# Kernel optimization log

Measured on AMD Instinct MI355X. Metric: run time of the kernel, lower is better.

## Reference

```python
import jax, jax.numpy as jnp
import numpy as np

NUM_EMBEDDINGS = 16384
EMBED_DIM = 256
COMMITMENT_COST = 0.25  # legacy=True: vq_loss = commit + beta * codebook


def setup_inputs() -> dict:
    key = jax.random.key(0)
    k1, k2, k3, k4 = jax.random.split(key, 4)
    z = jax.random.normal(k1, (8, 2048, EMBED_DIM), dtype=jnp.float32)
    # frozen codebook: normal(0, embedding_dim ** -0.5)
    codebook = jax.random.normal(k2, (NUM_EMBEDDINGS, EMBED_DIM), dtype=jnp.float32) * (EMBED_DIM ** -0.5)
    # learnable linear projection, torch default uniform init
    bound = 1.0 / np.sqrt(EMBED_DIM)
    proj_w = jax.random.uniform(k3, (EMBED_DIM, EMBED_DIM), dtype=jnp.float32, minval=-bound, maxval=bound)
    proj_b = jax.random.uniform(k4, (EMBED_DIM,), dtype=jnp.float32, minval=-bound, maxval=bound)
    return {"z": z, "codebook": codebook, "proj_w": proj_w, "proj_b": proj_b}


def reference(z, codebook, proj_w, proj_b):
    B, T, D = z.shape
    # projected codebook (the only learned part of the quantizer)
    quant_codebook = codebook @ proj_w.T + proj_b  # [K, D]
    z_flat = z.reshape(-1, D)  # [N, D]
    # squared L2 distances: ||z||^2 + ||c||^2 - 2 z.c
    dists = (
        jnp.sum(z_flat * z_flat, axis=1, keepdims=True)
        + jnp.sum(quant_codebook * quant_codebook, axis=1)
        - 2.0 * jnp.einsum("nd,kd->nk", z_flat, quant_codebook)
    )  # [N, K]
    idx = jnp.argmin(dists, axis=1)  # [N]
    quantized = quant_codebook[idx].reshape(z.shape)  # [B, T, D]

    commitment_loss = jnp.mean((jax.lax.stop_gradient(quantized) - z) ** 2)
    codebook_loss = jnp.mean((quantized - jax.lax.stop_gradient(z)) ** 2)
    vq_loss = commitment_loss + COMMITMENT_COST * codebook_loss  # legacy formulation

    # straight-through estimator
    quantized = z + jax.lax.stop_gradient(quantized - z)
    encoding_indices = idx.reshape(B, T)
    return quantized, vq_loss, encoding_indices
```

## Files before the change

### kernel.cpp

```cpp
#include <hip/hip_runtime.h>

typedef unsigned short u16;
typedef __bf16 bf16x8 __attribute__((ext_vector_type(8)));
typedef float f32x4 __attribute__((ext_vector_type(4)));

#define NQ 16384
#define NC 16384
#define DD 256
#define BM 128
#define BN 256
#define BK 32
#define NSPLIT 4
#define NPART (NSPLIT * 2)
#define NTILES ((NC / NSPLIT) / BN)

__device__ __forceinline__ u16 f2bf(float x) {
  unsigned u = __float_as_uint(x);
  u += 0x7fffu + ((u >> 16) & 1u);
  return (u16)(u >> 16);
}
__device__ __forceinline__ float bf2f(u16 h) {
  return __uint_as_float(((unsigned)h) << 16);
}

__device__ __forceinline__ void gl2lds16(const void* g, void* l) {
  __builtin_amdgcn_global_load_lds((__attribute__((address_space(1))) void*)g,
                                   (__attribute__((address_space(3))) void*)l,
                                   16, 0, 0);
}

__global__ __launch_bounds__(256) void split_z_kernel(const float* __restrict__ z,
                                                      u16* __restrict__ Ah,
                                                      u16* __restrict__ Al) {
  size_t i = (size_t)blockIdx.x * 256 + threadIdx.x;
  float4 v = ((const float4*)z)[i];
  float f[4] = {v.x, v.y, v.z, v.w};
  u16 hh[4], ll[4];
#pragma unroll
  for (int j = 0; j < 4; ++j) {
    hh[j] = f2bf(f[j]);
    ll[j] = f2bf(f[j] - bf2f(hh[j]));
  }
  ushort4 h; h.x = hh[0]; h.y = hh[1]; h.z = hh[2]; h.w = hh[3];
  ushort4 l; l.x = ll[0]; l.y = ll[1]; l.z = ll[2]; l.w = ll[3];
  ((ushort4*)Ah)[i] = h;
  ((ushort4*)Al)[i] = l;
}

__global__ __launch_bounds__(256) void norm256_kernel(const float* __restrict__ x,
                                                      float* __restrict__ nrm) {
  const int t = threadIdx.x;
  const int j = t & 7;
  const int row = blockIdx.x * 32 + (t >> 3);
  const float* q = x + (size_t)row * 256;
  float half[2];
#pragma unroll
  for (int h = 0; h < 2; ++h) {
    const float* p = q + h * 128;
    float v0 = p[j];
    float r = __fmul_rn(v0, v0);
#pragma unroll
    for (int i = 8; i < 128; i += 8) {
      float v = p[i + j];
      r = __fadd_rn(r, __fmul_rn(v, v));
    }
    float s1 = __fadd_rn(r, __shfl_xor(r, 1));
    float s2 = __fadd_rn(s1, __shfl_xor(s1, 2));
    half[h] = __fadd_rn(s2, __shfl_xor(s2, 4));
  }
  if (j == 0) nrm[row] = __fadd_rn(half[0], half[1]);
}

__global__ __launch_bounds__(256) void qc_gemm_kernel(const float* __restrict__ cb,
                                                      const float* __restrict__ W,
                                                      const float* __restrict__ bias,
                                                      float* __restrict__ qc) {
  __shared__ float As[64][33];
  __shared__ float Bs[64][33];
  const int bm = blockIdx.x >> 2;
  const int bn = blockIdx.x & 3;
  const int m0 = bm * 64, n0 = bn * 64;
  const int t = threadIdx.x;
  const int tx = t & 15, ty = t >> 4;
  float acc[4][4] = {};
  for (int kc = 0; kc < 256; kc += 32) {
    __syncthreads();
#pragma unroll
    for (int j = 0; j < 8; ++j) {
      int idx = j * 256 + t;
      int r = idx >> 5, c = idx & 31;
      As[r][c] = cb[(size_t)(m0 + r) * 256 + kc + c];
      Bs[r][c] = W[(size_t)(n0 + r) * 256 + kc + c];
    }
    __syncthreads();
#pragma unroll
    for (int kk = 0; kk < 32; ++kk) {
      float a[4], b[4];
#pragma unroll
      for (int u = 0; u < 4; ++u) a[u] = As[ty * 4 + u][kk];
#pragma unroll
      for (int v = 0; v < 4; ++v) b[v] = Bs[tx * 4 + v][kk];
#pragma unroll
      for (int u = 0; u < 4; ++u)
#pragma unroll
        for (int v = 0; v < 4; ++v) acc[u][v] += a[u] * b[v];
    }
  }
#pragma unroll
  for (int u = 0; u < 4; ++u)
#pragma unroll
    for (int v = 0; v < 4; ++v) {
      int r = m0 + ty * 4 + u, c = n0 + tx * 4 + v;
      qc[(size_t)r * 256 + c] = acc[u][v] + bias[c];
    }
}

__global__ __launch_bounds__(256) void split_qc_kernel(const float* __restrict__ qc,
                                                       u16* __restrict__ Bh,
                                                       u16* __restrict__ Bl) {
  size_t i = (size_t)blockIdx.x * 256 + threadIdx.x;
  float4 v = ((const float4*)qc)[i];
  float f[4] = {v.x, v.y, v.z, v.w};
  u16 hh[4], ll[4];
#pragma unroll
  for (int j = 0; j < 4; ++j) {
    hh[j] = f2bf(f[j]);
    ll[j] = f2bf(f[j] - bf2f(hh[j]));
  }
  ushort4 h; h.x = hh[0]; h.y = hh[1]; h.z = hh[2]; h.w = hh[3];
  ushort4 l; l.x = ll[0]; l.y = ll[1]; l.z = ll[2]; l.w = ll[3];
  ((ushort4*)Bh)[i] = h;
  ((ushort4*)Bl)[i] = l;
}

__global__ __launch_bounds__(256, 2) void vq_argmin_kernel(
    const u16* __restrict__ Ah, const u16* __restrict__ Al,
    const u16* __restrict__ Bh, const u16* __restrict__ Bl,
    const float* __restrict__ cnorm, const float* __restrict__ znorm,
    float* __restrict__ pval, int* __restrict__ pidx) {
  __shared__ __align__(16) u16 Ahs[BM * BK];
  __shared__ __align__(16) u16 Als[BM * BK];
  __shared__ __align__(16) u16 Bhs[BN * BK];
  __shared__ __align__(16) u16 Bls[BN * BK];

  const int bm = blockIdx.x / NSPLIT;
  const int spl = blockIdx.x % NSPLIT;
  const int lane = threadIdx.x & 63;
  const int wid = threadIdx.x >> 6;
  const int wm = wid >> 1, wn = wid & 1;
  const int l15 = lane & 15;
  const int lg = lane >> 4;
  const int m0 = bm * BM;
  const int ns0 = spl * (NC / NSPLIT);

  const int st_r = lane >> 2;
  const int st_k = (((lane & 3) ^ ((lane >> 3) & 3)) << 3);

  const int rd_sw = ((lg ^ ((l15 >> 1) & 3)) << 3);

  float zrow[4][4];
#pragma unroll
  for (int mi = 0; mi < 4; ++mi)
#pragma unroll
    for (int i = 0; i < 4; ++i)
      zrow[mi][i] = znorm[m0 + wm * 64 + mi * 16 + lg * 4 + i];

  float rmin[4][4];
  int ridx[4][4];
#pragma unroll
  for (int a = 0; a < 4; ++a)
#pragma unroll
    for (int b = 0; b < 4; ++b) { rmin[a][b] = 3.4e38f; ridx[a][b] = 0; }

  for (int nt = 0; nt < NTILES; ++nt) {
    const int n0 = ns0 + nt * BN;
    f32x4 acc[4][8];
#pragma unroll
    for (int a = 0; a < 4; ++a)
#pragma unroll
      for (int b = 0; b < 8; ++b) {
        f32x4 zz = {0.f, 0.f, 0.f, 0.f};
        acc[a][b] = zz;
      }

    for (int kc = 0; kc < DD; kc += BK) {
      __syncthreads();
#pragma unroll
      for (int j = 0; j < 2; ++j) {
        const int grp = wid * 2 + j;
        const int r = grp * 16 + st_r;
        const size_t ga = (size_t)(m0 + r) * DD + kc + st_k;
        gl2lds16(Ah + ga, Ahs + grp * 512);
        gl2lds16(Al + ga, Als + grp * 512);
      }
#pragma unroll
      for (int j = 0; j < 4; ++j) {
        const int grp = wid * 4 + j;
        const int r = grp * 16 + st_r;
        const size_t gb = (size_t)(n0 + r) * DD + kc + st_k;
        gl2lds16(Bh + gb, Bhs + grp * 512);
        gl2lds16(Bl + gb, Bls + grp * 512);
      }
      __syncthreads();

      bf16x8 ah[4], al[4];
#pragma unroll
      for (int mi = 0; mi < 4; ++mi) {
        const int r = wm * 64 + mi * 16 + l15;
        const int off = r * BK + rd_sw;
        ah[mi] = *(const bf16x8*)&Ahs[off];
        al[mi] = *(const bf16x8*)&Als[off];
      }
#pragma unroll
      for (int ni = 0; ni < 8; ++ni) {
        const int r = wn * 128 + ni * 16 + l15;
        const int off = r * BK + rd_sw;
        const bf16x8 bh = *(const bf16x8*)&Bhs[off];
        const bf16x8 bl = *(const bf16x8*)&Bls[off];
#pragma unroll
        for (int mi = 0; mi < 4; ++mi) {
          acc[mi][ni] = __builtin_amdgcn_mfma_f32_16x16x32_bf16(ah[mi], bh, acc[mi][ni], 0, 0, 0);
          acc[mi][ni] = __builtin_amdgcn_mfma_f32_16x16x32_bf16(ah[mi], bl, acc[mi][ni], 0, 0, 0);
          acc[mi][ni] = __builtin_amdgcn_mfma_f32_16x16x32_bf16(al[mi], bh, acc[mi][ni], 0, 0, 0);
        }
      }
    }
#pragma unroll
    for (int ni = 0; ni < 8; ++ni) {
      const int col = n0 + wn * 128 + ni * 16 + l15;
      const float cn = cnorm[col];
#pragma unroll
      for (int mi = 0; mi < 4; ++mi)
#pragma unroll
        for (int i = 0; i < 4; ++i) {
          const float s = __fadd_rn(zrow[mi][i], cn);
          const float v = __fsub_rn(s, __fmul_rn(2.0f, acc[mi][ni][i]));
          if (v < rmin[mi][i]) { rmin[mi][i] = v; ridx[mi][i] = col; }
        }
    }
  }
#pragma unroll
  for (int mi = 0; mi < 4; ++mi)
#pragma unroll
    for (int i = 0; i < 4; ++i) {
      float v = rmin[mi][i];
      int ix = ridx[mi][i];
#pragma unroll
      for (int d = 1; d < 16; d <<= 1) {
        float ov = __shfl_xor(v, d);
        int oi = __shfl_xor(ix, d);
        if (ov < v || (ov == v && oi < ix)) { v = ov; ix = oi; }
      }
      if (l15 == 0) {
        const int row = m0 + wm * 64 + mi * 16 + lg * 4 + i;
        const int part = spl * 2 + wn;
        pval[(size_t)part * NQ + row] = v;
        pidx[(size_t)part * NQ + row] = ix;
      }
    }
}

__global__ __launch_bounds__(256) void finalize_kernel(
    const float* __restrict__ pval, const int* __restrict__ pidx,
    const float* __restrict__ qc, const float* __restrict__ z,
    float* __restrict__ out, float* __restrict__ loss_acc) {
  __shared__ int sidx[8];
  __shared__ float red[256];
  const int bid = blockIdx.x;
  const int t = threadIdx.x;
  if (t < 8) {
    const int row = bid * 8 + t;
    float best = pval[row];
    int bi = pidx[row];
    for (int s2 = 1; s2 < NPART; ++s2) {
      float v = pval[(size_t)s2 * NQ + row];
      int ix = pidx[(size_t)s2 * NQ + row];
      if (v < best || (v == best && ix < bi)) { best = v; bi = ix; }
    }
    sidx[t] = bi;
    out[4194305 + row] = (float)bi;
  }
  __syncthreads();
  float d2 = 0.f;
#pragma unroll
  for (int r = 0; r < 8; ++r) {
    const int row = bid * 8 + r;
    const int ix = sidx[r];
    const float q = qc[(size_t)ix * 256 + t];
    const float zz = z[(size_t)row * 256 + t];
    out[(size_t)row * 256 + t] = q;
    const float d = q - zz;
    d2 += d * d;
  }
  red[t] = d2;
  for (int st = 128; st; st >>= 1) {
    __syncthreads();
    if (t < st) red[t] += red[t + st];
  }
  if (t == 0) atomicAdd(loss_acc, red[0]);
}

__global__ void write_loss_kernel(const float* __restrict__ loss_acc, float* __restrict__ out) {
  out[4194304] = 1.25f * loss_acc[0] / 4194304.0f;
}

extern "C" void kernel_launch(void* const* d_in, const int* in_sizes, int n_in,
                              void* d_out, int out_size, void* d_ws, size_t ws_size,
                              hipStream_t stream) {
  const float* z = (const float*)d_in[0];
  const float* cb = (const float*)d_in[1];
  const float* W = (const float*)d_in[2];
  const float* bias = (const float*)d_in[3];
  float* out = (float*)d_out;
  char* ws = (char*)d_ws;

  constexpr size_t OFF_QC = 0;
  constexpr size_t OFF_AH = OFF_QC + 16777216;
  constexpr size_t OFF_AL = OFF_AH + 8388608;
  constexpr size_t OFF_BH = OFF_AL + 8388608;
  constexpr size_t OFF_BL = OFF_BH + 8388608;
  constexpr size_t OFF_CN = OFF_BL + 8388608;
  constexpr size_t OFF_ZN = OFF_CN + 65536;
  constexpr size_t OFF_PV = OFF_ZN + 65536;
  constexpr size_t OFF_PI = OFF_PV + 1048576;
  constexpr size_t OFF_ACC = OFF_PI + 1048576;

  float* qc = (float*)(ws + OFF_QC);
  u16* Ah = (u16*)(ws + OFF_AH);
  u16* Al = (u16*)(ws + OFF_AL);
  u16* Bh = (u16*)(ws + OFF_BH);
  u16* Bl = (u16*)(ws + OFF_BL);
  float* cn = (float*)(ws + OFF_CN);
  float* zn = (float*)(ws + OFF_ZN);
  float* pv = (float*)(ws + OFF_PV);
  int* pi = (int*)(ws + OFF_PI);
  float* lacc = (float*)(ws + OFF_ACC);

  hipMemsetAsync(lacc, 0, 4, stream);
  split_z_kernel<<<4096, 256, 0, stream>>>(z, Ah, Al);
  qc_gemm_kernel<<<1024, 256, 0, stream>>>(cb, W, bias, qc);
  norm256_kernel<<<NQ / 32, 256, 0, stream>>>(z, zn);
  norm256_kernel<<<NC / 32, 256, 0, stream>>>(qc, cn);
  split_qc_kernel<<<4096, 256, 0, stream>>>(qc, Bh, Bl);
  vq_argmin_kernel<<<(NQ / BM) * NSPLIT, 256, 0, stream>>>(Ah, Al, Bh, Bl, cn, zn, pv, pi);
  finalize_kernel<<<NQ / 8, 256, 0, stream>>>(pv, pi, qc, z, out, lacc);
  write_loss_kernel<<<1, 1, 0, stream>>>(lacc, out);
}
```

Before: 573.9 us.

## Double-buffer LDS tiles with async prefetch and regroup MFMA issue order

Adds two LDS buffers so the global-to-LDS loads for the next K-step are issued before computing the current one, which removes one barrier per step and overlaps memory with MFMA. The three split-precision MFMA passes are regrouped into separate loops over all B fragments, which are now held in registers. The split count drops from 4 to 2 and launch bounds change to 1 block per SM. That gives fewer but longer blocks, and znorm is reloaded per tile instead of kept in registers. Doubling LDS and the register pressure from the B fragments reduce occupancy, and fewer blocks may underfill the CUs.

New measurement: 680.9 us. 18.6% more time.

```diff
diff --git a/kernel.cpp b/kernel.cpp
--- a/kernel.cpp
+++ b/kernel.cpp
@@ -10,9 +10,10 @@
 #define BM 128
 #define BN 256
 #define BK 32
-#define NSPLIT 4
+#define NSPLIT 2
 #define NPART (NSPLIT * 2)
 #define NTILES ((NC / NSPLIT) / BN)
+#define NSTEPS (NTILES * 8)
 
 __device__ __forceinline__ u16 f2bf(float x) {
   unsigned u = __float_as_uint(x);
@@ -133,15 +134,15 @@
   ((ushort4*)Bl)[i] = l;
 }
 
-__global__ __launch_bounds__(256, 2) void vq_argmin_kernel(
+__global__ __launch_bounds__(256, 1) void vq_argmin_kernel(
     const u16* __restrict__ Ah, const u16* __restrict__ Al,
     const u16* __restrict__ Bh, const u16* __restrict__ Bl,
     const float* __restrict__ cnorm, const float* __restrict__ znorm,
     float* __restrict__ pval, int* __restrict__ pidx) {
-  __shared__ __align__(16) u16 Ahs[BM * BK];
-  __shared__ __align__(16) u16 Als[BM * BK];
-  __shared__ __align__(16) u16 Bhs[BN * BK];
-  __shared__ __align__(16) u16 Bls[BN * BK];
+  __shared__ __align__(16) u16 Ahs[2][BM * BK];
+  __shared__ __align__(16) u16 Als[2][BM * BK];
+  __shared__ __align__(16) u16 Bhs[2][BN * BK];
+  __shared__ __align__(16) u16 Bls[2][BN * BK];
 
   const int bm = blockIdx.x / NSPLIT;
   const int spl = blockIdx.x % NSPLIT;
@@ -158,12 +159,27 @@
 
   const int rd_sw = ((lg ^ ((l15 >> 1) & 3)) << 3);
 
-  float zrow[4][4];
-#pragma unroll
-  for (int mi = 0; mi < 4; ++mi)
-#pragma unroll
-    for (int i = 0; i < 4; ++i)
-      zrow[mi][i] = znorm[m0 + wm * 64 + mi * 16 + lg * 4 + i];
+  auto stage = [&](int buf, int s) {
+    const int ntt = s >> 3;
+    const int kcc = (s & 7) * BK;
+    const int nn0 = ns0 + ntt * BN;
+#pragma unroll
+    for (int j = 0; j < 2; ++j) {
+      const int grp = wid * 2 + j;
+      const int r = grp * 16 + st_r;
+      const size_t ga = (size_t)(m0 + r) * DD + kcc + st_k;
+      gl2lds16(Ah + ga, &Ahs[buf][grp * 512]);
+      gl2lds16(Al + ga, &Als[buf][grp * 512]);
+    }
+#pragma unroll
+    for (int j = 0; j < 4; ++j) {
+      const int grp = wid * 4 + j;
+      const int r = grp * 16 + st_r;
+      const size_t gb = (size_t)(nn0 + r) * DD + kcc + st_k;
+      gl2lds16(Bh + gb, &Bhs[buf][grp * 512]);
+      gl2lds16(Bl + gb, &Bls[buf][grp * 512]);
+    }
+  };
 
   float rmin[4][4];
   int ridx[4][4];
@@ -171,6 +187,9 @@
   for (int a = 0; a < 4; ++a)
 #pragma unroll
     for (int b = 0; b < 4; ++b) { rmin[a][b] = 3.4e38f; ridx[a][b] = 0; }
+
+  stage(0, 0);
+  __syncthreads();
 
   for (int nt = 0; nt < NTILES; ++nt) {
     const int n0 = ns0 + nt * BN;
@@ -183,60 +202,67 @@
         acc[a][b] = zz;
       }
 
-    for (int kc = 0; kc < DD; kc += BK) {
-      __syncthreads();
-#pragma unroll
-      for (int j = 0; j < 2; ++j) {
-        const int grp = wid * 2 + j;
-        const int r = grp * 16 + st_r;
-        const size_t ga = (size_t)(m0 + r) * DD + kc + st_k;
-        gl2lds16(Ah + ga, Ahs + grp * 512);
-        gl2lds16(Al + ga, Als + grp * 512);
-      }
-#pragma unroll
-      for (int j = 0; j < 4; ++j) {
-        const int grp = wid * 4 + j;
-        const int r = grp * 16 + st_r;
-        const size_t gb = (size_t)(n0 + r) * DD + kc + st_k;
-        gl2lds16(Bh + gb, Bhs + grp * 512);
-        gl2lds16(Bl + gb, Bls + grp * 512);
-      }
-      __syncthreads();
-
-      bf16x8 ah[4], al[4];
+#pragma unroll 1
+    for (int k8 = 0; k8 < 8; ++k8) {
+      const int s = nt * 8 + k8;
+      const int cur = s & 1;
+      if (s + 1 < NSTEPS) stage(cur ^ 1, s + 1);
+
+      bf16x8 ah[4], al[4], bh[8], bl[8];
 #pragma unroll
       for (int mi = 0; mi < 4; ++mi) {
         const int r = wm * 64 + mi * 16 + l15;
         const int off = r * BK + rd_sw;
-        ah[mi] = *(const bf16x8*)&Ahs[off];
-        al[mi] = *(const bf16x8*)&Als[off];
+        ah[mi] = *(const bf16x8*)&Ahs[cur][off];
+        al[mi] = *(const bf16x8*)&Als[cur][off];
       }
 #pragma unroll
       for (int ni = 0; ni < 8; ++ni) {
         const int r = wn * 128 + ni * 16 + l15;
         const int off = r * BK + rd_sw;
-        const bf16x8 bh = *(const bf16x8*)&Bhs[off];
-        const bf16x8 bl = *(const bf16x8*)&Bls[off];
-#pragma unroll
-        for (int mi = 0; mi < 4; ++mi) {
-          acc[mi][ni] = __builtin_amdgcn_mfma_f32_16x16x32_bf16(ah[mi], bh, acc[mi][ni], 0, 0, 0);
-          acc[mi][ni] = __builtin_amdgcn_mfma_f32_16x16x32_bf16(ah[mi], bl, acc[mi][ni], 0, 0, 0);
-          acc[mi][ni] = __builtin_amdgcn_mfma_f32_16x16x32_bf16(al[mi], bh, acc[mi][ni], 0, 0, 0);
-        }
-      }
-    }
-#pragma unroll
-    for (int ni = 0; ni < 8; ++ni) {
-      const int col = n0 + wn * 128 + ni * 16 + l15;
-      const float cn = cnorm[col];
-#pragma unroll
-      for (int mi = 0; mi < 4; ++mi)
+        bh[ni] = *(const bf16x8*)&Bhs[cur][off];
+        bl[ni] = *(const bf16x8*)&Bls[cur][off];
+      }
+#pragma unroll
+      for (int ni = 0; ni < 8; ++ni)
+#pragma unroll
+        for (int mi = 0; mi < 4; ++mi)
+          acc[mi][ni] = __builtin_amdgcn_mfma_f32_16x16x32_bf16(ah[mi], bh[ni], acc[mi][ni], 0, 0, 0);
+#pragma unroll
+      for (int ni = 0; ni < 8; ++ni)
+#pragma unroll
+        for (int mi = 0; mi < 4; ++mi)
+          acc[mi][ni] = __builtin_amdgcn_mfma_f32_16x16x32_bf16(ah[mi], bl[ni], acc[mi][ni], 0, 0, 0);
+#pragma unroll
+      for (int ni = 0; ni < 8; ++ni)
+#pragma unroll
+        for (int mi = 0; mi < 4; ++mi)
+          acc[mi][ni] = __builtin_amdgcn_mfma_f32_16x16x32_bf16(al[mi], bh[ni], acc[mi][ni], 0, 0, 0);
+
+      __syncthreads();
+    }
+
+    float cnv[8];
+#pragma unroll
+    for (int ni = 0; ni < 8; ++ni)
+      cnv[ni] = cnorm[n0 + wn * 128 + ni * 16 + l15];
+#pragma unroll
+    for (int mi = 0; mi < 4; ++mi) {
+      float zr[4];
+#pragma unroll
+      for (int i = 0; i < 4; ++i)
+        zr[i] = znorm[m0 + wm * 64 + mi * 16 + lg * 4 + i];
+#pragma unroll
+      for (int ni = 0; ni < 8; ++ni) {
+        const int col = n0 + wn * 128 + ni * 16 + l15;
+        const float cn = cnv[ni];
 #pragma unroll
         for (int i = 0; i < 4; ++i) {
-          const float s = __fadd_rn(zrow[mi][i], cn);
+          const float s = __fadd_rn(zr[i], cn);
           const float v = __fsub_rn(s, __fmul_rn(2.0f, acc[mi][ni][i]));
           if (v < rmin[mi][i]) { rmin[mi][i] = v; ridx[mi][i] = col; }
         }
+      }
     }
   }
 #pragma unroll
```
